# Performance work log

Measured on AMD Instinct MI355X. Metric: run time of the kernel, lower is better.

Reference implementation:

```python
import jax, jax.numpy as jnp
import numpy as np
import math

B, S, H, NH = 1, 2048, 1024, 16  # batch, seq, hidden, heads


def setup_inputs() -> dict:
    key = jax.random.key(0)
    ks = jax.random.split(key, 12)
    inp = {
        "query": jax.random.normal(ks[0], (B, S, H), dtype=jnp.float32),
        "key": jax.random.normal(ks[1], (B, S, H), dtype=jnp.float32),
        "value": jax.random.normal(ks[2], (B, S, H), dtype=jnp.float32),
        "attention_mask": jax.random.randint(ks[3], (1, 1, S, S), 0, 2, dtype=jnp.int32),
        # torch nn.Linear params: y = x @ W.T + b, W init ~ U(-1/sqrt(H), 1/sqrt(H))
        "Wq": jax.random.uniform(ks[4], (H, H), jnp.float32, -1, 1) / math.sqrt(H),
        "bq": jax.random.uniform(ks[5], (H,), jnp.float32, -1, 1) / math.sqrt(H),
        "Wk": jax.random.uniform(ks[6], (H, H), jnp.float32, -1, 1) / math.sqrt(H),
        "bk": jax.random.uniform(ks[7], (H,), jnp.float32, -1, 1) / math.sqrt(H),
        "Wv": jax.random.uniform(ks[8], (H, H), jnp.float32, -1, 1) / math.sqrt(H),
        "bv": jax.random.uniform(ks[9], (H,), jnp.float32, -1, 1) / math.sqrt(H),
        "Wo": jax.random.uniform(ks[10], (H, H), jnp.float32, -1, 1) / math.sqrt(H),
        "bo": jax.random.uniform(ks[11], (H,), jnp.float32, -1, 1) / math.sqrt(H),
        "head": NH,
        "hidden_size": H,
    }
    return inp


def reference(query, key, value, attention_mask, Wq, bq, Wk, bk, Wv, bv, Wo, bo, head, hidden_size):
    b, s, _ = query.shape
    d_k = hidden_size // head

    def proj(x, W, bias):
        # [b, s, hidden] -> [b, head, s, d_k]
        y = x @ W.T + bias
        return y.reshape(b, s, head, d_k).transpose(0, 2, 1, 3)

    q = proj(query, Wq, bq)
    k = proj(key, Wk, bk)
    v = proj(value, Wv, bv)

    # naive full score matrix, as in the source (scale by sqrt(d_k) = last dim of q)
    scores = jnp.einsum("bhqd,bhkd->bhqk", q, k) / math.sqrt(d_k)
    # faithful quirk: masked positions are set to 0 (not -inf) before softmax
    scores = jnp.where(attention_mask == 0, jnp.zeros((), scores.dtype), scores)
    attn = jax.nn.softmax(scores, axis=-1)

    out = jnp.einsum("bhqk,bhkd->bhqd", attn, v)  # [b, head, s, d_k]
    out = out.transpose(0, 2, 1, 3).reshape(b, s, head * d_k)
    return out @ Wo.T + bo
```

## Files before the change

kernel.cpp:

```cpp
#include <hip/hip_runtime.h>
#include <hip/hip_bf16.h>


#define S_LEN 2048
#define HID   1024
#define NHEAD 16
#define DK    64

typedef unsigned short u16;
typedef __attribute__((ext_vector_type(8))) short bf16x8;
typedef __attribute__((ext_vector_type(4))) short bf16x4;
typedef __attribute__((ext_vector_type(4))) float f32x4;
typedef __attribute__((ext_vector_type(4))) unsigned u32x4;

__device__ __forceinline__ void load16_lds(const void* g, void* l) {
  __builtin_amdgcn_global_load_lds(
      (const __attribute__((address_space(1))) void*)g,
      (__attribute__((address_space(3))) void*)l, 16, 0, 0);
}

__device__ __forceinline__ short bfbits(float x) {
  __hip_bfloat16 h = __float2bfloat16(x);
  return *(short*)&h;
}
__device__ __forceinline__ bf16x8 cvt8(float4 a, float4 b) {
  bf16x8 r;
  r[0] = bfbits(a.x); r[1] = bfbits(a.y); r[2] = bfbits(a.z); r[3] = bfbits(a.w);
  r[4] = bfbits(b.x); r[5] = bfbits(b.y); r[6] = bfbits(b.z); r[7] = bfbits(b.w);
  return r;
}
__device__ __forceinline__ float bf2f(u16 u) {
  unsigned v = (unsigned)u << 16;
  return *(float*)&v;
}

__global__ __launch_bounds__(256) void cvt_pack_kernel(
    const float* __restrict__ q, const float* __restrict__ k,
    const float* __restrict__ v, const float* __restrict__ wq,
    const float* __restrict__ wk, const float* __restrict__ wv,
    const float* __restrict__ wo, const int* __restrict__ mask,
    u16* __restrict__ Xbf, u16* __restrict__ Wbf,
    unsigned int* __restrict__ bitsT) {
  const int y = blockIdx.y;
  if (y == 7) {
    if (blockIdx.x >= 512) return;
    int idx = blockIdx.x * 256 + threadIdx.x;
    int row = idx & 2047, widx = idx >> 11;
    const int4* p = (const int4*)(mask + (size_t)row * S_LEN + widx * 32);
    unsigned word = 0;
#pragma unroll
    for (int i = 0; i < 8; ++i) {
      int4 mv = p[i];
      word |= (unsigned)(mv.x != 0) << (i * 4 + 0);
      word |= (unsigned)(mv.y != 0) << (i * 4 + 1);
      word |= (unsigned)(mv.z != 0) << (i * 4 + 2);
      word |= (unsigned)(mv.w != 0) << (i * 4 + 3);
    }
    bitsT[(size_t)widx * S_LEN + row] = word;
    return;
  }
  size_t i = ((size_t)blockIdx.x * 256 + threadIdx.x) * 8;
  const float* src;
  u16* dst;
  size_t n;
  if (y < 3) {
    src = y == 0 ? q : (y == 1 ? k : v);
    dst = Xbf + (size_t)y * (S_LEN * HID);
    n = (size_t)S_LEN * HID;
  } else {
    int w = y - 3;
    src = w == 0 ? wq : (w == 1 ? wk : (w == 2 ? wv : wo));
    dst = Wbf + (size_t)w * (HID * HID);
    n = (size_t)HID * HID;
  }
  if (i >= n) return;
  float4 a = *(const float4*)(src + i);
  float4 b = *(const float4*)(src + i + 4);
  *(bf16x8*)(dst + i) = cvt8(a, b);
}

__global__ __launch_bounds__(256, 2) void gemm_qkv(
    const u16* __restrict__ Xbf, const u16* __restrict__ Wbf,
    const float* __restrict__ bq, const float* __restrict__ bk,
    const float* __restrict__ bv, u16* __restrict__ Qb,
    u16* __restrict__ Kb, u16* __restrict__ Vt) {
  constexpr int Mm = 2048, Kk = 1024, NIT = 16;
  const int tid = threadIdx.x, lane = tid & 63, wave = tid >> 6;
  const int q4 = lane >> 4, c16 = lane & 15;
  const int bx = blockIdx.x;
  const int xcd = bx & 7, s = bx >> 3;
  const int mBase = (s & 15) * 128;
  const int nG = xcd * 3 + (s >> 4);
  const int nBase = nG * 128;
  const int z = nBase >> 10;
  const u16* A = Xbf + (size_t)z * (S_LEN * HID);
  const float* bias = z == 0 ? bq : (z == 1 ? bk : bv);
  const float oscale = (z == 0) ? 0.125f * 1.44269504088896f : 1.0f;

  const int wr = wave >> 1, wc = wave & 1;

  __shared__ __align__(16) u16 As[2][2][128 * 32];
  __shared__ __align__(16) u16 Bs[2][2][128 * 32];

  f32x4 acc[4][4] = {};
  const int srow = lane >> 2;
  const int sx8 = ((lane & 3) ^ ((srow >> 1) & 3)) * 8;
  const int rx8 = (q4 ^ ((c16 >> 1) & 3)) * 8;

  auto issue = [&](int it, int buf) {
#pragma unroll
    for (int j = 0; j < 4; ++j) {
      int u = wave * 4 + j, h = u >> 3, grp = u & 7;
      load16_lds(A + (size_t)(mBase + grp * 16 + srow) * Kk + it * 64 +
                     h * 32 + sx8,
                 &As[buf][h][grp * 512]);
    }
#pragma unroll
    for (int j = 0; j < 4; ++j) {
      int u = wave * 4 + j, h = u >> 3, grp = u & 7;
      load16_lds(Wbf + (size_t)(nBase + grp * 16 + srow) * Kk + it * 64 +
                     h * 32 + sx8,
                 &Bs[buf][h][grp * 512]);
    }
  };

  issue(0, 0);
  __syncthreads();

  for (int it = 0; it < NIT; ++it) {
    const int buf = it & 1, nbuf = buf ^ 1;
    if (it + 1 < NIT) issue(it + 1, nbuf);
#pragma unroll
    for (int kk = 0; kk < 2; ++kk) {
      bf16x8 af[4], bfr[4];
#pragma unroll
      for (int t = 0; t < 4; ++t)
        af[t] = *(const bf16x8*)&As[buf][kk][(wr * 64 + t * 16 + c16) * 32 + rx8];
#pragma unroll
      for (int t = 0; t < 4; ++t)
        bfr[t] = *(const bf16x8*)&Bs[buf][kk][(wc * 64 + t * 16 + c16) * 32 + rx8];
#pragma unroll
      for (int mt = 0; mt < 4; ++mt)
#pragma unroll
        for (int nt = 0; nt < 4; ++nt)
          acc[mt][nt] = __builtin_amdgcn_mfma_f32_16x16x32_bf16(
              af[mt], bfr[nt], acc[mt][nt], 0, 0, 0);
    }
    __syncthreads();
  }

#pragma unroll
  for (int nt = 0; nt < 4; ++nt) {
    int colg = nBase + wc * 64 + nt * 16 + c16;
    int col = colg & 1023;
    float bv2 = bias[col];
#pragma unroll
    for (int mt = 0; mt < 4; ++mt) {
#pragma unroll
      for (int r = 0; r < 4; ++r) {
        int row = mBase + wr * 64 + mt * 16 + q4 * 4 + r;
        float v = (acc[mt][nt][r] + bv2) * oscale;
        if (z == 2) {
          int vv = row & 31;
          int rowp = (row & ~31) | (((vv & 15) << 1) | (vv >> 4));
          ((__hip_bfloat16*)Vt)[(size_t)col * Mm + rowp] = __float2bfloat16(v);
        } else {
          u16* C = z == 0 ? Qb : Kb;
          ((__hip_bfloat16*)C)[(size_t)row * 1024 + col] = __float2bfloat16(v);
        }
      }
    }
  }
}

__global__ __launch_bounds__(512, 4) void attn_kernel(
    const u16* __restrict__ Qb, const u16* __restrict__ Kb,
    const u16* __restrict__ Vt, const unsigned* __restrict__ mbT,
    u16* __restrict__ partOA, u16* __restrict__ partO3,
    float* __restrict__ partL) {
  constexpr int NITA = 8;
  const int lin = blockIdx.x + 8 * (blockIdx.y + 16 * blockIdx.z);
  const int work = ((lin & 7) << 6) | (lin >> 3);
  const int qt = work & 7, h = (work >> 3) & 15, zz = work >> 7;
  const int tid = threadIdx.x, lane = tid & 63, wave = tid >> 6;
  const int q4 = lane >> 4, c16 = lane & 15;

  __shared__ __align__(16) u16 Ks[2][2][64 * 32];
  __shared__ __align__(16) u16 Vs[2][2][64 * 32];
  __shared__ __align__(16) u16 Ps[8][32 * 72];

  const int q0 = qt * 256 + wave * 32;

  bf16x8 qf[2][2];
#pragma unroll
  for (int m = 0; m < 2; ++m)
#pragma unroll
    for (int kk = 0; kk < 2; ++kk)
      qf[m][kk] = *(const bf16x8*)(Qb + (size_t)(q0 + m * 16 + c16) * HID +
                                   h * DK + kk * 32 + q4 * 8);

  f32x4 o[2][4] = {};
  float l_lane[2][4] = {{}, {}};
  const unsigned mlo = 1u << c16, mhi = mlo << 16;

  const int srow = lane >> 2;
  const int sx8 = ((lane & 3) ^ ((srow >> 1) & 3)) * 8;
  const int rx8 = (q4 ^ ((c16 >> 1) & 3)) * 8;
  const int kvbase = zz * (S_LEN / 4);

  auto issueKV = [&](int it, int buf) {
    const int kv0 = kvbase + it * 64;
#pragma unroll
    for (int j = 0; j < 2; ++j) {
      int i = wave * 2 + j;
      if (i < 8) {
        int half = i >> 2, grp = i & 3;
        load16_lds(Kb + (size_t)(kv0 + grp * 16 + srow) * HID + h * DK +
                       half * 32 + sx8,
                   &Ks[buf][half][grp * 512]);
      } else {
        int ii = i - 8;
        int half = ii >> 2, grp = ii & 3;
        load16_lds(Vt + (size_t)(h * DK + grp * 16 + srow) * S_LEN + kv0 +
                       half * 32 + sx8,
                   &Vs[buf][half][grp * 512]);
      }
    }
  };

  issueKV(0, 0);
  __syncthreads();

  u16* pw = &Ps[wave][0];

  for (int it = 0; it < NITA; ++it) {
    const int buf = it & 1, nbuf = buf ^ 1;
    if (it + 1 < NITA) issueKV(it + 1, nbuf);

    const unsigned* mr = mbT + (size_t)(zz * 16 + it * 2) * S_LEN + q0 + q4 * 4;

#pragma unroll
    for (int ntp = 0; ntp < 2; ++ntp) {
      u32x4 mw0 = *(const u32x4*)(mr + (size_t)ntp * S_LEN);
      u32x4 mw1 = *(const u32x4*)(mr + (size_t)ntp * S_LEN + 16);
      f32x4 sv[2][2];
#pragma unroll
      for (int ntb = 0; ntb < 2; ++ntb) {
        const int nt = ntp * 2 + ntb;
        const int rsw = (nt * 16 + c16) * 32 + rx8;
        bf16x8 kf0 = *(const bf16x8*)&Ks[buf][0][rsw];
        bf16x8 kf1 = *(const bf16x8*)&Ks[buf][1][rsw];
#pragma unroll
        for (int m = 0; m < 2; ++m) {
          f32x4 a = {};
          a = __builtin_amdgcn_mfma_f32_16x16x32_bf16(qf[m][0], kf0, a, 0, 0, 0);
          a = __builtin_amdgcn_mfma_f32_16x16x32_bf16(qf[m][1], kf1, a, 0, 0, 0);
          sv[m][ntb] = a;
        }
      }
#pragma unroll
      for (int m = 0; m < 2; ++m) {
        const u32x4 mw = m ? mw1 : mw0;
#pragma unroll
        for (int r = 0; r < 4; ++r) {
          unsigned word = mw[r];
          float s0 = (word & mlo) ? sv[m][0][r] : 0.0f;
          float s1 = (word & mhi) ? sv[m][1][r] : 0.0f;
          float p0, p1;
          asm("v_exp_f32 %0, %1" : "=v"(p0) : "v"(s0));
          asm("v_exp_f32 %0, %1" : "=v"(p1) : "v"(s1));
          l_lane[m][r] += p0 + p1;
          unsigned pk;
          asm("v_cvt_pk_bf16_f32 %0, %1, %2" : "=v"(pk) : "v"(p0), "v"(p1));
          *(unsigned*)&pw[(m * 16 + q4 * 4 + r) * 72 + ntp * 32 + c16 * 2] = pk;
        }
      }
    }

    asm volatile("s_waitcnt lgkmcnt(0)" ::: "memory");

#pragma unroll
    for (int kk = 0; kk < 2; ++kk) {
      bf16x8 pa0 = *(const bf16x8*)&pw[(c16) * 72 + kk * 32 + q4 * 8];
      bf16x8 pa1 = *(const bf16x8*)&pw[(16 + c16) * 72 + kk * 32 + q4 * 8];
#pragma unroll
      for (int nt = 0; nt < 4; ++nt) {
        const int rsw = (nt * 16 + c16) * 32 + rx8;
        bf16x8 vb = *(const bf16x8*)&Vs[buf][kk][rsw];
        o[0][nt] = __builtin_amdgcn_mfma_f32_16x16x32_bf16(pa0, vb, o[0][nt], 0, 0, 0);
        o[1][nt] = __builtin_amdgcn_mfma_f32_16x16x32_bf16(pa1, vb, o[1][nt], 0, 0, 0);
      }
    }
    __syncthreads();
  }

  u16* pO = (zz < 3) ? (partOA + (size_t)zz * (S_LEN * HID)) : partO3;
#pragma unroll
  for (int m = 0; m < 2; ++m)
#pragma unroll
    for (int r = 0; r < 4; ++r) {
      float s = l_lane[m][r];
#pragma unroll
      for (int d = 1; d < 16; d <<= 1) s += __shfl_xor(s, d);
      int row = q0 + m * 16 + q4 * 4 + r;
#pragma unroll
      for (int nt = 0; nt < 4; ++nt)
        ((__hip_bfloat16*)pO)[(size_t)row * HID + h * DK + nt * 16 + c16] =
            __float2bfloat16(o[m][nt][r]);
      if (c16 == 0)
        partL[((size_t)zz * NHEAD + h) * S_LEN + row] = s;
    }
}

__global__ __launch_bounds__(256) void gemm_out(
    const u16* __restrict__ pOA, const u16* __restrict__ pO3,
    const float* __restrict__ partL, const u16* __restrict__ Wo,
    const float* __restrict__ bo, float* __restrict__ out) {
  constexpr int Nn = 1024, Kk = 1024, NIT = 16;
  constexpr size_t M2 = (size_t)S_LEN * HID;
  const int tid = threadIdx.x, lane = tid & 63, wave = tid >> 6;
  const int q4 = lane >> 4, c16 = lane & 15;
  const int bx = blockIdx.x;
  const int xcd = bx & 7, s = bx >> 3;
  const int mBase = (xcd * 8 + (s & 7)) * 32;
  const int nBase = (s >> 3) * 128;
  const int wn = wave * 32;

  __shared__ __align__(16) u16 As[2][2][32 * 32];
  __shared__ __align__(16) u16 Bs[2][2][128 * 32];
  __shared__ float linv[32][16];

  f32x4 acc[2][2] = {};
  const int srow = lane >> 2;
  const int sx8 = ((lane & 3) ^ ((srow >> 1) & 3)) * 8;
  const int rx8 = (q4 ^ ((c16 >> 1) & 3)) * 8;

  const int arow = tid >> 3, acu = tid & 7;
  const int ahalf = acu >> 2;
  const int aoff = arow * 32 + ((acu & 3) ^ ((arow >> 1) & 3)) * 8;

  auto issueB = [&](int it, int buf) {
#pragma unroll
    for (int j = 0; j < 4; ++j) {
      int u = wave * 4 + j, h = u >> 3, grp = u & 7;
      load16_lds(Wo + (size_t)(nBase + grp * 16 + srow) * Kk + it * 64 +
                     h * 32 + sx8,
                 &Bs[buf][h][grp * 512]);
    }
  };

  bf16x8 av0, av1, av2, av3;
  auto aload = [&](int it) {
    const u16* p = pOA + (size_t)(mBase + arow) * Kk + it * 64 + acu * 8;
    av0 = *(const bf16x8*)p;
    av1 = *(const bf16x8*)(p + M2);
    av2 = *(const bf16x8*)(p + 2 * M2);
    av3 = *(const bf16x8*)(pO3 + (size_t)(mBase + arow) * Kk + it * 64 + acu * 8);
  };
  auto awrite = [&](int it, int buf) {
    float inv = linv[arow][it];
    bf16x8 r;
#pragma unroll
    for (int j = 0; j < 8; ++j) {
      float v = (bf2f((u16)av0[j]) + bf2f((u16)av1[j]) +
                 bf2f((u16)av2[j]) + bf2f((u16)av3[j])) * inv;
      r[j] = bfbits(v);
    }
    *(bf16x8*)&As[buf][ahalf][aoff] = r;
  };

#pragma unroll
  for (int e = 0; e < 2; ++e) {
    int idx = tid * 2 + e, row = idx >> 4, hh = idx & 15;
    float l = 0.0f;
#pragma unroll
    for (int z = 0; z < 4; ++z)
      l += partL[(size_t)(z * NHEAD + hh) * S_LEN + mBase + row];
    linv[row][hh] = 1.0f / l;
  }
  aload(0);
  issueB(0, 0);
  __syncthreads();
  awrite(0, 0);
  __syncthreads();

  for (int it = 0; it < NIT; ++it) {
    const int buf = it & 1, nbuf = buf ^ 1;
    if (it + 1 < NIT) { aload(it + 1); issueB(it + 1, nbuf); }
#pragma unroll
    for (int kk = 0; kk < 2; ++kk) {
      bf16x8 af[2], bfr[2];
#pragma unroll
      for (int t = 0; t < 2; ++t)
        af[t] = *(const bf16x8*)&As[buf][kk][(t * 16 + c16) * 32 + rx8];
#pragma unroll
      for (int t = 0; t < 2; ++t)
        bfr[t] = *(const bf16x8*)&Bs[buf][kk][(wn + t * 16 + c16) * 32 + rx8];
#pragma unroll
      for (int mt = 0; mt < 2; ++mt)
#pragma unroll
        for (int nt = 0; nt < 2; ++nt)
          acc[mt][nt] = __builtin_amdgcn_mfma_f32_16x16x32_bf16(
              af[mt], bfr[nt], acc[mt][nt], 0, 0, 0);
    }
    if (it + 1 < NIT) awrite(it + 1, nbuf);
    __syncthreads();
  }

#pragma unroll
  for (int nt = 0; nt < 2; ++nt) {
    int col = nBase + wn + nt * 16 + c16;
    float bv = bo[col];
#pragma unroll
    for (int mt = 0; mt < 2; ++mt)
#pragma unroll
      for (int r = 0; r < 4; ++r) {
        int row = mBase + mt * 16 + q4 * 4 + r;
        out[(size_t)row * Nn + col] = acc[mt][nt][r] + bv;
      }
  }
}

extern "C" void kernel_launch(void* const* d_in, const int* in_sizes, int n_in,
                              void* d_out, int out_size, void* d_ws, size_t ws_size,
                              hipStream_t stream) {
  const float* q    = (const float*)d_in[0];
  const float* k    = (const float*)d_in[1];
  const float* v    = (const float*)d_in[2];
  const int*   mask = (const int*)d_in[3];
  const float* Wq = (const float*)d_in[4];
  const float* bq = (const float*)d_in[5];
  const float* Wk = (const float*)d_in[6];
  const float* bk = (const float*)d_in[7];
  const float* Wv = (const float*)d_in[8];
  const float* bv = (const float*)d_in[9];
  const float* Wo = (const float*)d_in[10];
  const float* bo = (const float*)d_in[11];

  const size_t M2 = (size_t)S_LEN * HID;
  const size_t W1 = (size_t)HID * HID;
  const size_t need = (4 * W1 + 3 * M2 + 3 * M2) * 2 +
                      (size_t)S_LEN * 64 * 4 + 2 * NHEAD * S_LEN * 4;
  if (ws_size < need) return;

  u16* Wbf = (u16*)d_ws;
  u16* Xbf = Wbf + 4 * W1;
  u16* Qb = Xbf + 3 * M2;
  u16* Kb = Qb + M2;
  u16* Vt = Kb + M2;
  unsigned* mbits = (unsigned*)(Vt + M2);
  u16* partOA = Xbf;
  u16* partO3 = Wbf;
  float* partL = (float*)(Wbf + 2 * W1);

  hipLaunchKernelGGL(cvt_pack_kernel, dim3(1024, 8), dim3(256), 0, stream,
                     q, k, v, Wq, Wk, Wv, Wo, mask, Xbf, Wbf, mbits);

  hipLaunchKernelGGL(gemm_qkv, dim3(384), dim3(256), 0, stream,
                     Xbf, Wbf, bq, bk, bv, Qb, Kb, Vt);

  hipLaunchKernelGGL(attn_kernel, dim3(S_LEN / 256, NHEAD, 4), dim3(512), 0,
                     stream, Qb, Kb, Vt, mbits, partOA, partO3, partL);

  hipLaunchKernelGGL(gemm_out, dim3(512), dim3(256), 0, stream,
                     partOA, partO3, partL, Wbf + 3 * W1, bo, (float*)d_out);
}
```

Baseline: 210.5 us.

## Shrink QKV GEMM N-tile, add MFMA priority hints, deepen out-GEMM A prefetch

The QKV projection GEMM drops its N tile from 128 to 64, doubling the grid to 768 blocks and raising the launch-bounds occupancy hint to 3. The aim is better CU fill and more latency hiding, at the cost of lower per-block data reuse. The attention kernel wraps its MFMA sections in s_setprio so matrix work gets issue priority over the softmax and exp code of other waves. The output GEMM double-buffers its register prefetch of partial attention outputs, loading two iterations ahead to hide global latency, which adds register pressure.

New measurement: 201.7 us. 1.04x faster.

```diff
diff --git a/kernel.cpp b/kernel.cpp
--- a/kernel.cpp
+++ b/kernel.cpp
@@ -79,7 +79,7 @@
   *(bf16x8*)(dst + i) = cvt8(a, b);
 }
 
-__global__ __launch_bounds__(256, 2) void gemm_qkv(
+__global__ __launch_bounds__(256, 3) void gemm_qkv(
     const u16* __restrict__ Xbf, const u16* __restrict__ Wbf,
     const float* __restrict__ bq, const float* __restrict__ bk,
     const float* __restrict__ bv, u16* __restrict__ Qb,
@@ -90,8 +90,8 @@
   const int bx = blockIdx.x;
   const int xcd = bx & 7, s = bx >> 3;
   const int mBase = (s & 15) * 128;
-  const int nG = xcd * 3 + (s >> 4);
-  const int nBase = nG * 128;
+  const int nG = xcd * 6 + (s >> 4);
+  const int nBase = nG * 64;
   const int z = nBase >> 10;
   const u16* A = Xbf + (size_t)z * (S_LEN * HID);
   const float* bias = z == 0 ? bq : (z == 1 ? bk : bv);
@@ -100,9 +100,9 @@
   const int wr = wave >> 1, wc = wave & 1;
 
   __shared__ __align__(16) u16 As[2][2][128 * 32];
-  __shared__ __align__(16) u16 Bs[2][2][128 * 32];
-
-  f32x4 acc[4][4] = {};
+  __shared__ __align__(16) u16 Bs[2][2][64 * 32];
+
+  f32x4 acc[4][2] = {};
   const int srow = lane >> 2;
   const int sx8 = ((lane & 3) ^ ((srow >> 1) & 3)) * 8;
   const int rx8 = (q4 ^ ((c16 >> 1) & 3)) * 8;
@@ -116,8 +116,8 @@
                  &As[buf][h][grp * 512]);
     }
 #pragma unroll
-    for (int j = 0; j < 4; ++j) {
-      int u = wave * 4 + j, h = u >> 3, grp = u & 7;
+    for (int j = 0; j < 2; ++j) {
+      int u = wave * 2 + j, h = u >> 2, grp = u & 3;
       load16_lds(Wbf + (size_t)(nBase + grp * 16 + srow) * Kk + it * 64 +
                      h * 32 + sx8,
                  &Bs[buf][h][grp * 512]);
@@ -132,17 +132,17 @@
     if (it + 1 < NIT) issue(it + 1, nbuf);
 #pragma unroll
     for (int kk = 0; kk < 2; ++kk) {
-      bf16x8 af[4], bfr[4];
+      bf16x8 af[4], bfr[2];
 #pragma unroll
       for (int t = 0; t < 4; ++t)
         af[t] = *(const bf16x8*)&As[buf][kk][(wr * 64 + t * 16 + c16) * 32 + rx8];
 #pragma unroll
-      for (int t = 0; t < 4; ++t)
-        bfr[t] = *(const bf16x8*)&Bs[buf][kk][(wc * 64 + t * 16 + c16) * 32 + rx8];
+      for (int t = 0; t < 2; ++t)
+        bfr[t] = *(const bf16x8*)&Bs[buf][kk][(wc * 32 + t * 16 + c16) * 32 + rx8];
 #pragma unroll
       for (int mt = 0; mt < 4; ++mt)
 #pragma unroll
-        for (int nt = 0; nt < 4; ++nt)
+        for (int nt = 0; nt < 2; ++nt)
           acc[mt][nt] = __builtin_amdgcn_mfma_f32_16x16x32_bf16(
               af[mt], bfr[nt], acc[mt][nt], 0, 0, 0);
     }
@@ -150,8 +150,8 @@
   }
 
 #pragma unroll
-  for (int nt = 0; nt < 4; ++nt) {
-    int colg = nBase + wc * 64 + nt * 16 + c16;
+  for (int nt = 0; nt < 2; ++nt) {
+    int colg = nBase + wc * 32 + nt * 16 + c16;
     int col = colg & 1023;
     float bv2 = bias[col];
 #pragma unroll
@@ -244,6 +244,7 @@
       u32x4 mw0 = *(const u32x4*)(mr + (size_t)ntp * S_LEN);
       u32x4 mw1 = *(const u32x4*)(mr + (size_t)ntp * S_LEN + 16);
       f32x4 sv[2][2];
+      __builtin_amdgcn_s_setprio(1);
 #pragma unroll
       for (int ntb = 0; ntb < 2; ++ntb) {
         const int nt = ntp * 2 + ntb;
@@ -258,6 +259,7 @@
           sv[m][ntb] = a;
         }
       }
+      __builtin_amdgcn_s_setprio(0);
 #pragma unroll
       for (int m = 0; m < 2; ++m) {
         const u32x4 mw = m ? mw1 : mw0;
@@ -279,6 +281,7 @@
 
     asm volatile("s_waitcnt lgkmcnt(0)" ::: "memory");
 
+    __builtin_amdgcn_s_setprio(1);
 #pragma unroll
     for (int kk = 0; kk < 2; ++kk) {
       bf16x8 pa0 = *(const bf16x8*)&pw[(c16) * 72 + kk * 32 + q4 * 8];
@@ -291,6 +294,7 @@
         o[1][nt] = __builtin_amdgcn_mfma_f32_16x16x32_bf16(pa1, vb, o[1][nt], 0, 0, 0);
       }
     }
+    __builtin_amdgcn_s_setprio(0);
     __syncthreads();
   }
 
@@ -349,21 +353,21 @@
     }
   };
 
-  bf16x8 av0, av1, av2, av3;
-  auto aload = [&](int it) {
+  bf16x8 avA[4], avB[4];
+  auto aloadTo = [&](bf16x8* dst, int it) {
     const u16* p = pOA + (size_t)(mBase + arow) * Kk + it * 64 + acu * 8;
-    av0 = *(const bf16x8*)p;
-    av1 = *(const bf16x8*)(p + M2);
-    av2 = *(const bf16x8*)(p + 2 * M2);
-    av3 = *(const bf16x8*)(pO3 + (size_t)(mBase + arow) * Kk + it * 64 + acu * 8);
+    dst[0] = *(const bf16x8*)p;
+    dst[1] = *(const bf16x8*)(p + M2);
+    dst[2] = *(const bf16x8*)(p + 2 * M2);
+    dst[3] = *(const bf16x8*)(pO3 + (size_t)(mBase + arow) * Kk + it * 64 + acu * 8);
   };
-  auto awrite = [&](int it, int buf) {
+  auto awriteFrom = [&](const bf16x8* src, int it, int buf) {
     float inv = linv[arow][it];
     bf16x8 r;
 #pragma unroll
     for (int j = 0; j < 8; ++j) {
-      float v = (bf2f((u16)av0[j]) + bf2f((u16)av1[j]) +
-                 bf2f((u16)av2[j]) + bf2f((u16)av3[j])) * inv;
+      float v = (bf2f((u16)src[0][j]) + bf2f((u16)src[1][j]) +
+                 bf2f((u16)src[2][j]) + bf2f((u16)src[3][j])) * inv;
       r[j] = bfbits(v);
     }
     *(bf16x8*)&As[buf][ahalf][aoff] = r;
@@ -378,15 +382,17 @@
       l += partL[(size_t)(z * NHEAD + hh) * S_LEN + mBase + row];
     linv[row][hh] = 1.0f / l;
   }
-  aload(0);
+  aloadTo(avA, 0);
   issueB(0, 0);
   __syncthreads();
-  awrite(0, 0);
+  awriteFrom(avA, 0, 0);
+  aloadTo(avB, 1);
   __syncthreads();
 
   for (int it = 0; it < NIT; ++it) {
     const int buf = it & 1, nbuf = buf ^ 1;
-    if (it + 1 < NIT) { aload(it + 1); issueB(it + 1, nbuf); }
+    if (it + 1 < NIT) issueB(it + 1, nbuf);
+    if (it + 2 < NIT) aloadTo((it & 1) ? avB : avA, it + 2);
 #pragma unroll
     for (int kk = 0; kk < 2; ++kk) {
       bf16x8 af[2], bfr[2];
@@ -403,7 +409,7 @@
           acc[mt][nt] = __builtin_amdgcn_mfma_f32_16x16x32_bf16(
               af[mt], bfr[nt], acc[mt][nt], 0, 0, 0);
     }
-    if (it + 1 < NIT) awrite(it + 1, nbuf);
+    if (it + 1 < NIT) awriteFrom((it & 1) ? avA : avB, it + 1, nbuf);
     __syncthreads();
   }
 
@@ -456,7 +462,7 @@
   hipLaunchKernelGGL(cvt_pack_kernel, dim3(1024, 8), dim3(256), 0, stream,
                      q, k, v, Wq, Wk, Wv, Wo, mask, Xbf, Wbf, mbits);
 
-  hipLaunchKernelGGL(gemm_qkv, dim3(384), dim3(256), 0, stream,
+  hipLaunchKernelGGL(gemm_qkv, dim3(768), dim3(256), 0, stream,
                      Xbf, Wbf, bq, bk, bv, Qb, Kb, Vt);
 
   hipLaunchKernelGGL(attn_kernel, dim3(S_LEN / 256, NHEAD, 4), dim3(512), 0,
```
